# Optimization experiments

Hardware: AMD Instinct MI355X
Metric: run time of the kernel (lower is better)

The kernel has to match this reference:

```python
import jax, jax.numpy as jnp
import numpy as np

N, D, K, L = 65536, 512, 1024, 4
TEMPERATURE = 1.0


def setup_inputs() -> dict:
    key = jax.random.key(0)
    k1, k2 = jax.random.split(key)
    inputs = jax.random.normal(k1, (N, D), dtype=jnp.float32)
    # L separate (non-shared) codebooks, first n_embed rows of each nn.Embedding
    # (the extra padding row is never selected by argmin, so we omit it).
    codebooks = jax.random.normal(k2, (L, K, D), dtype=jnp.float32) * 0.02
    return {"inputs": inputs, "codebooks": codebooks}


def _quantize_level(residual, cb):
    # addmm-based squared-distance: ||r||^2 + ||c||^2 - 2 r @ c^T, then / temperature
    r_sq = jnp.sum(residual * residual, axis=-1, keepdims=True)        # [N,1]
    c_sq = jnp.sum(cb * cb, axis=-1)[None, :]                          # [1,K]
    dists = (r_sq + c_sq - 2.0 * jnp.einsum('nd,kd->nk', residual, cb)) / TEMPERATURE
    idx = jnp.argmin(dists, axis=-1)                                   # [N]
    embeds = cb[idx]                                                   # [N,D] gather
    return embeds, idx


def reference(inputs, codebooks):
    """Residual quantization: sequentially quantize the residual with each
    level's codebook (eval-mode forward: no EMA buffer updates).
    Returns (quantized, codes) where quantized = sum of per-level embeds."""
    residual = inputs
    quant = jnp.zeros_like(inputs)
    codes = []
    for l in range(codebooks.shape[0]):  # L is small and fixed
        embeds, idx = _quantize_level(residual, codebooks[l])
        quant = quant + embeds
        residual = residual - embeds
        codes.append(idx)
    codes = jnp.stack(codes, axis=-1)  # [N, L] int32
    return quant, codes
```

## Files before the change

kernel.cpp:

```cpp
#include <hip/hip_runtime.h>

#define NROWS_TOTAL 65536
#define DDIM 512
#define KCODES 1024
#define LLEV 4
#define ROWS 32
#define KT 512
#define CODES_OFF ((size_t)NROWS_TOTAL * DDIM)
#define MARGIN 0.0625f

typedef __attribute__((address_space(1))) const unsigned int glb_u32_t;
typedef __attribute__((address_space(3))) unsigned int lds_u32_t;
typedef __attribute__((ext_vector_type(8))) short bf16x8;
typedef __attribute__((ext_vector_type(4))) float f32x4;

__device__ __forceinline__ void gload_lds16(const void* g, void* l) {
  __builtin_amdgcn_global_load_lds((glb_u32_t*)g, (lds_u32_t*)l, 16, 0, 0);
}

__device__ __forceinline__ unsigned short f2bf(float f) {
  union { float f; unsigned u; } c; c.f = f;
  return (unsigned short)((c.u + 0x7fffu + ((c.u >> 16) & 1u)) >> 16);
}
__device__ __forceinline__ float bf2f(short h) {
  union { unsigned u; float f; } c; c.u = ((unsigned)(unsigned short)h) << 16;
  return c.f;
}
__device__ __forceinline__ bf16x8 packbf8(float4 a, float4 b) {
  bf16x8 r;
  r[0] = (short)f2bf(a.x); r[1] = (short)f2bf(a.y);
  r[2] = (short)f2bf(a.z); r[3] = (short)f2bf(a.w);
  r[4] = (short)f2bf(b.x); r[5] = (short)f2bf(b.y);
  r[6] = (short)f2bf(b.z); r[7] = (short)f2bf(b.w);
  return r;
}

__global__ void csq_kernel(const float* __restrict__ cb, float* __restrict__ csq) {
  int row  = blockIdx.x * 4 + (threadIdx.x >> 6);
  int lane = threadIdx.x & 63;
  const float* p = cb + (size_t)row * DDIM;
  float s = 0.f;
#pragma unroll
  for (int i = 0; i < 8; ++i) { float v = p[lane + 64 * i]; s = fmaf(v, v, s); }
#pragma unroll
  for (int off = 32; off > 0; off >>= 1) s += __shfl_down(s, off, 64);
  if (lane == 0) csq[row] = s;
}

__global__ void pack_kernel(const float* __restrict__ cb, unsigned short* __restrict__ cbB) {
  const int gid = blockIdx.x * 256 + threadIdx.x;
  const int g = gid & 3, ks = (gid >> 2) & 15, c = (gid >> 6) & 1023, l = gid >> 16;
  const float* p = cb + ((size_t)(l * KCODES + c)) * DDIM + ks * 32 + g * 8;
  float4 v0 = *(const float4*)p, v1 = *(const float4*)(p + 4);
  bf16x8 r = packbf8(v0, v1);
  *(bf16x8*)(cbB + ((((size_t)(l * 16 + ks) * 64 + (c >> 4)) * 4 + g) * 16 + (c & 15)) * 8) = r;
}

__launch_bounds__(256, 2)
__global__ void rq_mfma(const float* __restrict__ x, const float* __restrict__ cb,
                        const float* __restrict__ csq,
                        const unsigned short* __restrict__ cbB,
                        float* __restrict__ out) {
  __shared__ __align__(16) unsigned short ls_b[2][4096];
  __shared__ __align__(16) float ls_csq[1024];
  __shared__ unsigned long long ls_flags[64][16];
  __shared__ int ls_mi[64];
  __shared__ int ls_cnt[64];
  __shared__ int ls_hist[LLEV][64];

  const int tid = threadIdx.x;
  const int w = tid >> 6, lane = tid & 63;
  const int g = lane >> 4, c15 = lane & 15;
  const int rowbase = blockIdx.x * 64;
  const int arow_g = rowbase + w * 16 + c15;

  bf16x8 areg[16];
#pragma unroll
  for (int ks = 0; ks < 16; ++ks) {
    const float* p = x + (size_t)arow_g * DDIM + ks * 32 + g * 8;
    float4 v0 = *(const float4*)p, v1 = *(const float4*)(p + 4);
    areg[ks] = packbf8(v0, v1);
  }

  auto issue = [&](int lvl, int t, int buf) {
    const int ksn = t & 15, cgn = t >> 4;
    const unsigned short* src = cbB + (size_t)lvl * 524288 + ksn * 32768 + cgn * 4096
                                + w * 1024 + lane * 8;
    unsigned short* dst = &ls_b[buf][w * 1024 + lane * 8];
    gload_lds16(src, dst);
    gload_lds16(src + 512, dst + 512);
  };

  for (int l = 0; l < LLEV; ++l) {
    *(float4*)&ls_csq[tid * 4] = *(const float4*)(csq + l * KCODES + tid * 4);

    float mv[4]; int mi[4]; unsigned long long flg[4];
#pragma unroll
    for (int i = 0; i < 4; ++i) { mv[i] = 3.4e38f; mi[i] = 0; flg[i] = 0ull; }

    if (l == 0) issue(0, 0, 0);

    f32x4 acc[8];
    for (int cg = 0; cg < 8; ++cg) {
#pragma unroll
      for (int ks = 0; ks < 16; ++ks) {
        const int buf = ks & 1;
        __syncthreads();
        const int t = cg * 16 + ks;
        if (t < 127) issue(l, t + 1, buf ^ 1);
        else if (l < LLEV - 1) issue(l + 1, 0, buf ^ 1);

        if (ks == 0) {
#pragma unroll
          for (int f = 0; f < 8; ++f) acc[f] = (f32x4){0.f, 0.f, 0.f, 0.f};
        }
#pragma unroll
        for (int f = 0; f < 8; ++f) {
          bf16x8 bB = *(const bf16x8*)&ls_b[buf][f * 512 + g * 128 + c15 * 8];
          acc[f] = __builtin_amdgcn_mfma_f32_16x16x32_bf16(areg[ks], bB, acc[f], 0, 0, 0);
        }

        if (ks == 15) {
          float qv[8][4];
#pragma unroll
          for (int f = 0; f < 8; ++f) {
            float cs = ls_csq[cg * 128 + f * 16 + c15];
#pragma unroll
            for (int i = 0; i < 4; ++i) qv[f][i] = fmaf(-2.0f, acc[f][i], cs);
          }
#pragma unroll
          for (int i = 0; i < 4; ++i) {
            float lv = qv[0][i]; int li = cg * 128 + c15;
#pragma unroll
            for (int f = 1; f < 8; ++f) {
              int code = cg * 128 + f * 16 + c15;
              if (qv[f][i] < lv) { lv = qv[f][i]; li = code; }
            }
#pragma unroll
            for (int off = 1; off < 16; off <<= 1) {
              float ov = __shfl_xor(lv, off, 64);
              int oi = __shfl_xor(li, off, 64);
              if (ov < lv || (ov == lv && oi < li)) { lv = ov; li = oi; }
            }
            if (lv < mv[i] || (lv == mv[i] && li < mi[i])) { mv[i] = lv; mi[i] = li; }
            float thr = mv[i] + MARGIN;
#pragma unroll
            for (int f = 0; f < 8; ++f)
              if (qv[f][i] <= thr) flg[i] |= (1ull << (cg * 8 + f));
          }
        }
      }
    }

    const int row0 = w * 16 + g * 4;
#pragma unroll
    for (int i = 0; i < 4; ++i) {
      int cnt = __popcll(flg[i]);
#pragma unroll
      for (int off = 1; off < 16; off <<= 1) cnt += __shfl_xor(cnt, off, 64);
      ls_flags[row0 + i][c15] = flg[i];
      if (c15 == 0) { ls_mi[row0 + i] = mi[i]; ls_cnt[row0 + i] = cnt; }
    }

    for (int r = 0; r < 16; ++r) {
      const int row = w * 16 + r;
      if (ls_cnt[row] > 1) {
        const int grow = rowbase + row;
        const float* xp = x + (size_t)grow * DDIM + lane * 8;
        float4 a0 = *(const float4*)xp;
        float4 a1 = *(const float4*)(xp + 4);
        float rs0 = a0.x, rs1 = a0.y, rs2 = a0.z, rs3 = a0.w;
        float rs4 = a1.x, rs5 = a1.y, rs6 = a1.z, rs7 = a1.w;
        for (int lp = 0; lp < l; ++lp) {
          const float* cp = cb + ((size_t)(lp * KCODES + ls_hist[lp][row])) * DDIM + lane * 8;
          float4 e0 = *(const float4*)cp;
          float4 e1 = *(const float4*)(cp + 4);
          rs0 -= e0.x; rs1 -= e0.y; rs2 -= e0.z; rs3 -= e0.w;
          rs4 -= e1.x; rs5 -= e1.y; rs6 -= e1.z; rs7 -= e1.w;
        }
        float pr = 0.f;
        pr = fmaf(rs0, rs0, pr); pr = fmaf(rs1, rs1, pr);
        pr = fmaf(rs2, rs2, pr); pr = fmaf(rs3, rs3, pr);
        pr = fmaf(rs4, rs4, pr); pr = fmaf(rs5, rs5, pr);
        pr = fmaf(rs6, rs6, pr); pr = fmaf(rs7, rs7, pr);
#pragma unroll
        for (int off = 1; off < 64; off <<= 1) pr += __shfl_xor(pr, off, 64);
        float bs = 3.4e38f; int bc = 0x7fffffff;
        for (int j16 = 0; j16 < 16; ++j16) {
          unsigned long long b = ls_flags[row][j16];
          while (b) {
            int bit = __builtin_ctzll(b); b &= b - 1;
            int code = ((bit >> 3) << 7) + ((bit & 7) << 4) + j16;
            const float* cp = cb + ((size_t)(l * KCODES + code)) * DDIM + lane * 8;
            float4 e0 = *(const float4*)cp;
            float4 e1 = *(const float4*)(cp + 4);
            float pd = 0.f;
            pd = fmaf(rs0, e0.x, pd); pd = fmaf(rs1, e0.y, pd);
            pd = fmaf(rs2, e0.z, pd); pd = fmaf(rs3, e0.w, pd);
            pd = fmaf(rs4, e1.x, pd); pd = fmaf(rs5, e1.y, pd);
            pd = fmaf(rs6, e1.z, pd); pd = fmaf(rs7, e1.w, pd);
#pragma unroll
            for (int off = 1; off < 64; off <<= 1) pd += __shfl_xor(pd, off, 64);
            float s = (pr + ls_csq[code]) - 2.0f * pd;
            if (s < bs || (s == bs && code < bc)) { bs = s; bc = code; }
          }
        }
        if (lane == 0) ls_mi[row] = bc;
      }
    }
    __syncthreads();

    if (tid < 64) {
      int c = ls_mi[tid];
      ls_hist[l][tid] = c;
      out[CODES_OFF + (size_t)(rowbase + tid) * LLEV + l] = (float)c;
    }
    if (l < LLEV - 1) {
      const int idxr = ls_mi[w * 16 + c15];
      const float* crow = cb + ((size_t)(l * KCODES + idxr)) * DDIM;
#pragma unroll
      for (int ks = 0; ks < 16; ++ks) {
        const float* p = crow + ks * 32 + g * 8;
        float4 v0 = *(const float4*)p, v1 = *(const float4*)(p + 4);
        bf16x8 a = areg[ks];
        float4 n0, n1;
        n0.x = bf2f(a[0]) - v0.x; n0.y = bf2f(a[1]) - v0.y;
        n0.z = bf2f(a[2]) - v0.z; n0.w = bf2f(a[3]) - v0.w;
        n1.x = bf2f(a[4]) - v1.x; n1.y = bf2f(a[5]) - v1.y;
        n1.z = bf2f(a[6]) - v1.z; n1.w = bf2f(a[7]) - v1.w;
        areg[ks] = packbf8(n0, n1);
      }
    }
  }

  __syncthreads();
  {
    const int row = tid >> 2;
    const int d0 = (tid & 3) * 128;
    const float* p0 = cb + ((size_t)(0 * KCODES + ls_hist[0][row])) * DDIM + d0;
    const float* p1 = cb + ((size_t)(1 * KCODES + ls_hist[1][row])) * DDIM + d0;
    const float* p2 = cb + ((size_t)(2 * KCODES + ls_hist[2][row])) * DDIM + d0;
    const float* p3 = cb + ((size_t)(3 * KCODES + ls_hist[3][row])) * DDIM + d0;
    float* op = out + (size_t)(rowbase + row) * DDIM + d0;
#pragma unroll 8
    for (int ch = 0; ch < 32; ++ch) {
      float4 e0 = *(const float4*)(p0 + ch * 4);
      float4 e1 = *(const float4*)(p1 + ch * 4);
      float4 e2 = *(const float4*)(p2 + ch * 4);
      float4 e3 = *(const float4*)(p3 + ch * 4);
      float4 q;
      q.x = ((e0.x + e1.x) + e2.x) + e3.x;
      q.y = ((e0.y + e1.y) + e2.y) + e3.y;
      q.z = ((e0.z + e1.z) + e2.z) + e3.z;
      q.w = ((e0.w + e1.w) + e2.w) + e3.w;
      *(float4*)(op + ch * 4) = q;
    }
  }
}

#define DC 16
#define RSTRIDE 20

__launch_bounds__(256, 2)
__global__ void rq_kernel(const float* __restrict__ x, const float* __restrict__ cb,
                          const float* __restrict__ csq, float* __restrict__ out) {
  __shared__ float ls_cbT[DC * KT];
  __shared__ float ls_r[ROWS * RSTRIDE];
  __shared__ float ls_minv[ROWS * 64];
  __shared__ int   ls_mini[ROWS * 64];
  __shared__ float ls_rsqp[ROWS * 8];
  __shared__ float ls_rsq[ROWS];
  __shared__ int   ls_idx[ROWS];

  const int tid = threadIdx.x;
  const int rg  = tid >> 6;
  const int kg  = tid & 63;
  const int own_row = tid >> 3;
  const int own_d0  = (tid & 7) * 64;
  const int rowbase = blockIdx.x * ROWS;

  float rres[64];
  {
    const float4* xp = (const float4*)(x + (size_t)(rowbase + own_row) * DDIM + own_d0);
#pragma unroll
    for (int i = 0; i < 16; ++i) {
      float4 v = xp[i];
      rres[4*i] = v.x; rres[4*i+1] = v.y; rres[4*i+2] = v.z; rres[4*i+3] = v.w;
    }
  }

  for (int l = 0; l < LLEV; ++l) {
    {
      float p = 0.f;
#pragma unroll
      for (int i = 0; i < 64; ++i) p = fmaf(rres[i], rres[i], p);
      ls_rsqp[own_row * 8 + (tid & 7)] = p;
    }
    __syncthreads();
    if (tid < ROWS) {
      float s = 0.f;
#pragma unroll
      for (int i = 0; i < 8; ++i) s += ls_rsqp[tid * 8 + i];
      ls_rsq[tid] = s;
    }

    float mv[8]; int mi[8];
#pragma unroll
    for (int r = 0; r < 8; ++r) { mv[r] = 3.4e38f; mi[r] = 0; }

    const float* cbl = cb + (size_t)l * KCODES * DDIM;

    for (int kt = 0; kt < KCODES / KT; ++kt) {
      float acc[8][8];
#pragma unroll
      for (int r = 0; r < 8; ++r)
#pragma unroll
        for (int c = 0; c < 8; ++c) acc[r][c] = 0.f;

      for (int dc = 0; dc < DDIM / DC; ++dc) {
        __syncthreads();
        {
          int krow = tid >> 2;
          int dcol = (tid & 3) * 4;
#pragma unroll
          for (int p = 0; p < 8; ++p) {
            int klocal = p * 64 + krow;
            float4 v = *(const float4*)(cbl + (size_t)(kt * KT + klocal) * DDIM + dc * DC + dcol);
            ls_cbT[(dcol + 0) * KT + klocal] = v.x;
            ls_cbT[(dcol + 1) * KT + klocal] = v.y;
            ls_cbT[(dcol + 2) * KT + klocal] = v.z;
            ls_cbT[(dcol + 3) * KT + klocal] = v.w;
          }
        }
        if ((tid & 7) == (dc >> 2)) {
          switch (dc & 3) {
            case 0:
#pragma unroll
              for (int i = 0; i < 4; ++i)
                *(float4*)&ls_r[own_row * RSTRIDE + i * 4] =
                  make_float4(rres[0*16+4*i], rres[0*16+4*i+1], rres[0*16+4*i+2], rres[0*16+4*i+3]);
              break;
            case 1:
#pragma unroll
              for (int i = 0; i < 4; ++i)
                *(float4*)&ls_r[own_row * RSTRIDE + i * 4] =
                  make_float4(rres[1*16+4*i], rres[1*16+4*i+1], rres[1*16+4*i+2], rres[1*16+4*i+3]);
              break;
            case 2:
#pragma unroll
              for (int i = 0; i < 4; ++i)
                *(float4*)&ls_r[own_row * RSTRIDE + i * 4] =
                  make_float4(rres[2*16+4*i], rres[2*16+4*i+1], rres[2*16+4*i+2], rres[2*16+4*i+3]);
              break;
            default:
#pragma unroll
              for (int i = 0; i < 4; ++i)
                *(float4*)&ls_r[own_row * RSTRIDE + i * 4] =
                  make_float4(rres[3*16+4*i], rres[3*16+4*i+1], rres[3*16+4*i+2], rres[3*16+4*i+3]);
              break;
          }
        }
        __syncthreads();
        for (int ds4 = 0; ds4 < DC / 4; ++ds4) {
          float rvf[4][8];
#pragma unroll
          for (int r = 0; r < 8; ++r) {
            float4 t = *(const float4*)&ls_r[(rg * 8 + r) * RSTRIDE + ds4 * 4];
            rvf[0][r] = t.x; rvf[1][r] = t.y; rvf[2][r] = t.z; rvf[3][r] = t.w;
          }
#pragma unroll
          for (int jj = 0; jj < 4; ++jj) {
            float4 cv0 = *(const float4*)&ls_cbT[(ds4 * 4 + jj) * KT + 4 * kg];
            float4 cv1 = *(const float4*)&ls_cbT[(ds4 * 4 + jj) * KT + KT / 2 + 4 * kg];
#pragma unroll
            for (int r = 0; r < 8; ++r) {
              float rv = rvf[jj][r];
              acc[r][0] = fmaf(rv, cv0.x, acc[r][0]);
              acc[r][1] = fmaf(rv, cv0.y, acc[r][1]);
              acc[r][2] = fmaf(rv, cv0.z, acc[r][2]);
              acc[r][3] = fmaf(rv, cv0.w, acc[r][3]);
              acc[r][4] = fmaf(rv, cv1.x, acc[r][4]);
              acc[r][5] = fmaf(rv, cv1.y, acc[r][5]);
              acc[r][6] = fmaf(rv, cv1.z, acc[r][6]);
              acc[r][7] = fmaf(rv, cv1.w, acc[r][7]);
            }
          }
        }
      }
#pragma unroll
      for (int g = 0; g < 2; ++g)
#pragma unroll
        for (int c = 0; c < 4; ++c) {
          int k = kt * KT + g * (KT / 2) + 4 * kg + c;
          float cs = csq[l * KCODES + k];
#pragma unroll
          for (int r = 0; r < 8; ++r) {
            float s = (ls_rsq[rg * 8 + r] + cs) - 2.0f * acc[r][g * 4 + c];
            if (s < mv[r]) { mv[r] = s; mi[r] = k; }
          }
        }
    }

#pragma unroll
    for (int r = 0; r < 8; ++r) {
      ls_minv[(rg * 8 + r) * 64 + kg] = mv[r];
      ls_mini[(rg * 8 + r) * 64 + kg] = mi[r];
    }
    __syncthreads();
    if (tid < ROWS) {
      float bv = ls_minv[tid * 64]; int bi = ls_mini[tid * 64];
      for (int i = 1; i < 64; ++i) {
        float v = ls_minv[tid * 64 + i]; int ii = ls_mini[tid * 64 + i];
        if (v < bv || (v == bv && ii < bi)) { bv = v; bi = ii; }
      }
      ls_idx[tid] = bi;
      out[CODES_OFF + (size_t)(rowbase + tid) * LLEV + l] = (float)bi;
    }
    __syncthreads();
    {
      int idx = ls_idx[own_row];
      const float4* cp = (const float4*)(cbl + (size_t)idx * DDIM + own_d0);
#pragma unroll
      for (int i = 0; i < 16; ++i) {
        float4 v = cp[i];
        rres[4*i]   -= v.x; rres[4*i+1] -= v.y;
        rres[4*i+2] -= v.z; rres[4*i+3] -= v.w;
      }
    }
  }

  {
    const float4* xp = (const float4*)(x + (size_t)(rowbase + own_row) * DDIM + own_d0);
    float4* op = (float4*)(out + (size_t)(rowbase + own_row) * DDIM + own_d0);
#pragma unroll
    for (int i = 0; i < 16; ++i) {
      float4 v = xp[i];
      op[i] = make_float4(v.x - rres[4*i],   v.y - rres[4*i+1],
                          v.z - rres[4*i+2], v.w - rres[4*i+3]);
    }
  }
}

extern "C" void kernel_launch(void* const* d_in, const int* in_sizes, int n_in,
                              void* d_out, int out_size, void* d_ws, size_t ws_size,
                              hipStream_t stream) {
  const float* x  = (const float*)d_in[0];
  const float* cb = (const float*)d_in[1];
  float* out = (float*)d_out;
  float* csq = (float*)d_ws;
  unsigned short* cbB = (unsigned short*)((float*)d_ws + 4096);

  const size_t need = 4096 * sizeof(float)
                    + (size_t)LLEV * 16 * 64 * 4 * 16 * 8 * sizeof(unsigned short);

  csq_kernel<<<dim3((LLEV * KCODES) / 4), dim3(256), 0, stream>>>(cb, csq);
  if (ws_size >= need) {
    pack_kernel<<<dim3(1024), dim3(256), 0, stream>>>(cb, cbB);
    rq_mfma<<<dim3(NROWS_TOTAL / 64), dim3(256), 0, stream>>>(x, cb, csq, cbB, out);
  } else {
    rq_kernel<<<dim3(NROWS_TOTAL / ROWS), dim3(256), 0, stream>>>(x, cb, csq, out);
  }
}
```

Measured before the change: 1.378 ms.

## Deepen codebook LDS pipeline to six buffers with explicit vmcnt waits

Replaces the double-buffered codebook tile stream, which had a full __syncthreads per k-slice, with a six-slot LDS ring. Each iteration consumes two k-slices and keeps four chunks in flight, using explicit s_waitcnt vmcnt plus raw s_barrier in place of the full sync. This aims to hide global-to-LDS latency and halve barrier count. Cross-level prefetch is dropped: each level now restarts its pipeline. LDS use per block triples, which may limit occupancy at two blocks per CU.

```diff
diff --git a/kernel.cpp b/kernel.cpp
--- a/kernel.cpp
+++ b/kernel.cpp
@@ -61,7 +61,7 @@
                         const float* __restrict__ csq,
                         const unsigned short* __restrict__ cbB,
                         float* __restrict__ out) {
-  __shared__ __align__(16) unsigned short ls_b[2][4096];
+  __shared__ __align__(16) unsigned short ls_b[6][4096];
   __shared__ __align__(16) float ls_csq[1024];
   __shared__ unsigned long long ls_flags[64][16];
   __shared__ int ls_mi[64];
@@ -82,10 +82,9 @@
     areg[ks] = packbf8(v0, v1);
   }
 
-  auto issue = [&](int lvl, int t, int buf) {
-    const int ksn = t & 15, cgn = t >> 4;
-    const unsigned short* src = cbB + (size_t)lvl * 524288 + ksn * 32768 + cgn * 4096
-                                + w * 1024 + lane * 8;
+  auto issue_chunk = [&](int lvl, int t, int buf) {
+    const unsigned short* src = cbB + (size_t)lvl * 524288 + (size_t)(t & 15) * 32768
+                                + (size_t)(t >> 4) * 4096 + w * 1024 + lane * 8;
     unsigned short* dst = &ls_b[buf][w * 1024 + lane * 8];
     gload_lds16(src, dst);
     gload_lds16(src + 512, dst + 512);
@@ -93,61 +92,72 @@
 
   for (int l = 0; l < LLEV; ++l) {
     *(float4*)&ls_csq[tid * 4] = *(const float4*)(csq + l * KCODES + tid * 4);
+    asm volatile("s_waitcnt lgkmcnt(0)" ::: "memory");
 
     float mv[4]; int mi[4]; unsigned long long flg[4];
 #pragma unroll
     for (int i = 0; i < 4; ++i) { mv[i] = 3.4e38f; mi[i] = 0; flg[i] = 0ull; }
 
-    if (l == 0) issue(0, 0, 0);
+    issue_chunk(l, 0, 0); issue_chunk(l, 1, 1);
+    issue_chunk(l, 2, 2); issue_chunk(l, 3, 3);
 
     f32x4 acc[8];
-    for (int cg = 0; cg < 8; ++cg) {
-#pragma unroll
-      for (int ks = 0; ks < 16; ++ks) {
-        const int buf = ks & 1;
-        __syncthreads();
-        const int t = cg * 16 + ks;
-        if (t < 127) issue(l, t + 1, buf ^ 1);
-        else if (l < LLEV - 1) issue(l + 1, 0, buf ^ 1);
-
-        if (ks == 0) {
-#pragma unroll
-          for (int f = 0; f < 8; ++f) acc[f] = (f32x4){0.f, 0.f, 0.f, 0.f};
-        }
+    for (int u = 0; u < 64; ++u) {
+      const int cg = u >> 3, kk = u & 7;
+
+      if (u < 63) asm volatile("s_waitcnt vmcnt(4)" ::: "memory");
+      else        asm volatile("s_waitcnt vmcnt(0)" ::: "memory");
+      __builtin_amdgcn_s_barrier();
+      __builtin_amdgcn_sched_barrier(0);
+
+      if (u < 62) {
+        issue_chunk(l, 2 * u + 4, (2 * u + 4) % 6);
+        issue_chunk(l, 2 * u + 5, (2 * u + 5) % 6);
+      }
+
+      if (kk == 0) {
+#pragma unroll
+        for (int f = 0; f < 8; ++f) acc[f] = (f32x4){0.f, 0.f, 0.f, 0.f};
+      }
+
+      const int b0 = (2 * u) % 6;
+      const unsigned short* cb0 = &ls_b[b0][g * 128 + c15 * 8];
+      const unsigned short* cb1 = &ls_b[b0 + 1][g * 128 + c15 * 8];
+#pragma unroll
+      for (int f = 0; f < 8; ++f) {
+        bf16x8 bB0 = *(const bf16x8*)(cb0 + f * 512);
+        acc[f] = __builtin_amdgcn_mfma_f32_16x16x32_bf16(areg[2 * kk], bB0, acc[f], 0, 0, 0);
+        bf16x8 bB1 = *(const bf16x8*)(cb1 + f * 512);
+        acc[f] = __builtin_amdgcn_mfma_f32_16x16x32_bf16(areg[2 * kk + 1], bB1, acc[f], 0, 0, 0);
+      }
+
+      if (kk == 7) {
+        float qv[8][4];
 #pragma unroll
         for (int f = 0; f < 8; ++f) {
-          bf16x8 bB = *(const bf16x8*)&ls_b[buf][f * 512 + g * 128 + c15 * 8];
-          acc[f] = __builtin_amdgcn_mfma_f32_16x16x32_bf16(areg[ks], bB, acc[f], 0, 0, 0);
-        }
-
-        if (ks == 15) {
-          float qv[8][4];
-#pragma unroll
-          for (int f = 0; f < 8; ++f) {
-            float cs = ls_csq[cg * 128 + f * 16 + c15];
-#pragma unroll
-            for (int i = 0; i < 4; ++i) qv[f][i] = fmaf(-2.0f, acc[f][i], cs);
-          }
-#pragma unroll
-          for (int i = 0; i < 4; ++i) {
-            float lv = qv[0][i]; int li = cg * 128 + c15;
-#pragma unroll
-            for (int f = 1; f < 8; ++f) {
-              int code = cg * 128 + f * 16 + c15;
-              if (qv[f][i] < lv) { lv = qv[f][i]; li = code; }
-            }
-#pragma unroll
-            for (int off = 1; off < 16; off <<= 1) {
-              float ov = __shfl_xor(lv, off, 64);
-              int oi = __shfl_xor(li, off, 64);
-              if (ov < lv || (ov == lv && oi < li)) { lv = ov; li = oi; }
-            }
-            if (lv < mv[i] || (lv == mv[i] && li < mi[i])) { mv[i] = lv; mi[i] = li; }
-            float thr = mv[i] + MARGIN;
-#pragma unroll
-            for (int f = 0; f < 8; ++f)
-              if (qv[f][i] <= thr) flg[i] |= (1ull << (cg * 8 + f));
-          }
+          float cs = ls_csq[cg * 128 + f * 16 + c15];
+#pragma unroll
+          for (int i = 0; i < 4; ++i) qv[f][i] = fmaf(-2.0f, acc[f][i], cs);
+        }
+#pragma unroll
+        for (int i = 0; i < 4; ++i) {
+          float lv = qv[0][i]; int li = cg * 128 + c15;
+#pragma unroll
+          for (int f = 1; f < 8; ++f) {
+            int code = cg * 128 + f * 16 + c15;
+            if (qv[f][i] < lv) { lv = qv[f][i]; li = code; }
+          }
+#pragma unroll
+          for (int off = 1; off < 16; off <<= 1) {
+            float ov = __shfl_xor(lv, off, 64);
+            int oi = __shfl_xor(li, off, 64);
+            if (ov < lv || (ov == lv && oi < li)) { lv = ov; li = oi; }
+          }
+          if (lv < mv[i] || (lv == mv[i] && li < mi[i])) { mv[i] = lv; mi[i] = li; }
+          float thr = mv[i] + MARGIN;
+#pragma unroll
+          for (int f = 0; f < 8; ++f)
+            if (qv[f][i] <= thr) flg[i] |= (1ull << (cg * 8 + f));
         }
       }
     }
```

After: 1.737 ms. 1.26x slower.
